# Kernel optimization log

Hardware: AMD Instinct MI355X
Metric: run time of the kernel (lower is better)

Reference implementation:

```python
import jax, jax.numpy as jnp
import numpy as np

N_NODES = 50000
N_EDGES = 600000
D_IN = 128
D_OUT = 128


def setup_inputs() -> dict:
    key = jax.random.key(0)
    k1, k2, k3, k4 = jax.random.split(key, 4)
    mpg_ft = jax.random.normal(k1, (N_NODES, D_IN), dtype=jnp.float32)
    edge_index = jax.random.randint(k2, (2, N_EDGES), 0, N_NODES, dtype=jnp.int64)
    # GCNConv linear params (PyG: glorot weight [in, out], zero bias)
    limit = (6.0 / (D_IN + D_OUT)) ** 0.5
    W = jax.random.uniform(k3, (D_IN, D_OUT), dtype=jnp.float32, minval=-limit, maxval=limit)
    b = jnp.zeros((D_OUT,), dtype=jnp.float32)
    return {"mpg_ft": mpg_ft, "edge_index": edge_index, "W": W, "b": b}


def gcn_conv(x, edge_index, W, b):
    n = x.shape[0]
    # add self-loops (PyG GCNConv default)
    loops = jnp.arange(n, dtype=edge_index.dtype)
    src = jnp.concatenate([edge_index[0], loops])
    dst = jnp.concatenate([edge_index[1], loops])
    # symmetric normalization: deg computed on destination with unit edge weights
    deg = jax.ops.segment_sum(jnp.ones_like(dst, dtype=x.dtype), dst, num_segments=n)
    dis = jnp.where(deg > 0, jax.lax.rsqrt(jnp.maximum(deg, 1.0)), 0.0)
    norm = dis[src] * dis[dst]                      # [E+N]
    h = x @ W                                        # [N, D_OUT]
    msg = h[src] * norm[:, None]                     # [E+N, D_OUT] gather
    out = jax.ops.segment_sum(msg, dst, num_segments=n)  # scatter-add
    return out + b


def reference(mpg_ft, edge_index, W, b):
    # freeze=True: x = g.mpg_ft; conv=True: x = GCNConv(x, edge_index)
    return gcn_conv(mpg_ft, edge_index, W, b)
```

## Files before the change

### kernel.cpp

```cpp
#include <hip/hip_runtime.h>

#define D 128
#define CAP 64
#define BINCAP 4096
#define BINSHIFT 8

typedef __bf16 bf16x8 __attribute__((ext_vector_type(8)));
typedef float f32x4 __attribute__((ext_vector_type(4)));

static __device__ __forceinline__ unsigned short f2bf(float x) {
    unsigned int u = __builtin_bit_cast(unsigned int, x);
    unsigned int r = u + 0x7fffu + ((u >> 16) & 1u);
    return (unsigned short)(r >> 16);
}
static __device__ __forceinline__ float bitf(unsigned int u) {
    return __builtin_bit_cast(float, u);
}

__global__ __launch_bounds__(256) void prep_kernel(const float* __restrict__ W,
                                                   unsigned int* __restrict__ bincur,
                                                   unsigned short* __restrict__ wt, int NB) {
    int tid = blockIdx.x * 256 + threadIdx.x;
    int stride = gridDim.x * 256;
    if (tid < NB) bincur[tid] = (unsigned)tid * BINCAP;
    for (int i = tid; i < D * D; i += stride) {
        int r = i >> 7, c = i & 127;
        wt[c * 128 + r] = f2bf(W[i]);
    }
}

__global__ __launch_bounds__(256) void binA_kernel(const int* __restrict__ ei,
                                                   unsigned int* __restrict__ bincur,
                                                   unsigned int* __restrict__ binned, int E,
                                                   int NB) {
    __shared__ unsigned int hist[256];
    __shared__ unsigned int base[256];
    int t = threadIdx.x;
    int chunk = (E + gridDim.x - 1) / gridDim.x;
    int s0 = blockIdx.x * chunk, s1 = min(E, s0 + chunk);
    const int* dstp = ei + E;

    hist[t] = 0u;
    __syncthreads();
    for (int e = s0 + t; e < s1; e += 256) atomicAdd(&hist[dstp[e] >> BINSHIFT], 1u);
    __syncthreads();
    if (t < NB && hist[t]) base[t] = atomicAdd(&bincur[t], hist[t]);
    __syncthreads();
    hist[t] = 0u;
    __syncthreads();
    for (int e = s0 + t; e < s1; e += 256) {
        int src = ei[e];
        int d = dstp[e];
        int bin = d >> BINSHIFT;
        unsigned int off = atomicAdd(&hist[bin], 1u);
        binned[base[bin] + off] = ((unsigned)d << 16) | (unsigned)src;
    }
}

__global__ __launch_bounds__(256) void binB_kernel(const unsigned int* __restrict__ binned,
                                                   const unsigned int* __restrict__ bincur,
                                                   unsigned int* __restrict__ cnt,
                                                   unsigned short* __restrict__ bucket, int n) {
    __shared__ unsigned int lcnt[256];
    int t = threadIdx.x;
    int b = blockIdx.x;
    lcnt[t] = 0u;
    __syncthreads();
    unsigned int cstart = (unsigned)b * BINCAP;
    int m = (int)(bincur[b] - cstart);
    for (int i = t; i < m; i += 256) {
        unsigned int p = binned[cstart + i];
        unsigned int src = p & 0xffffu;
        unsigned int d = p >> 16;
        unsigned int slot = atomicAdd(&lcnt[d & 255u], 1u);
        bucket[(size_t)d * CAP + (slot & (CAP - 1))] = (unsigned short)src;
    }
    __syncthreads();
    int node = (b << BINSHIFT) + t;
    if (node < n) cnt[node] = lcnt[t];
}

__global__ __launch_bounds__(256) void mfma_gemm(const float* __restrict__ x,
                                                 const unsigned short* __restrict__ wt,
                                                 const unsigned int* __restrict__ cnt,
                                                 unsigned short* __restrict__ hs, int n) {
    __shared__ uint4 Xs[64 * 16];
    __shared__ uint4 Ws[128 * 16];
    int t = threadIdx.x;
    int rowbase = blockIdx.x * 64;

    const uint4* wg = (const uint4*)wt;
#pragma unroll
    for (int j = 0; j < 8; ++j) {
        int gi = t + j * 256;
        int r = gi >> 4, s = gi & 15;
        Ws[r * 16 + (s ^ (r & 7))] = wg[gi];
    }
    const float4* x4 = (const float4*)x;
#pragma unroll
    for (int j = 0; j < 4; ++j) {
        int gi = t + j * 256;
        int r = gi >> 4, s = gi & 15;
        uint4 v = make_uint4(0u, 0u, 0u, 0u);
        int grow = rowbase + r;
        if (grow < n) {
            float4 f0 = x4[(size_t)grow * 32 + s * 2];
            float4 f1 = x4[(size_t)grow * 32 + s * 2 + 1];
            v.x = f2bf(f0.x) | ((unsigned)f2bf(f0.y) << 16);
            v.y = f2bf(f0.z) | ((unsigned)f2bf(f0.w) << 16);
            v.z = f2bf(f1.x) | ((unsigned)f2bf(f1.y) << 16);
            v.w = f2bf(f1.z) | ((unsigned)f2bf(f1.w) << 16);
        }
        Xs[r * 16 + (s ^ (r & 7))] = v;
    }
    __syncthreads();

    int w = t >> 6, l = t & 63;
    int lr = l & 15, lg = l >> 4;
    f32x4 acc[4][2] = {};

#pragma unroll
    for (int kt = 0; kt < 4; ++kt) {
        int ks = kt * 4 + lg;
        bf16x8 bfr[2];
#pragma unroll
        for (int ct = 0; ct < 2; ++ct) {
            int nc = w * 32 + ct * 16 + lr;
            bfr[ct] = __builtin_bit_cast(bf16x8, Ws[nc * 16 + (ks ^ (nc & 7))]);
        }
#pragma unroll
        for (int mt = 0; mt < 4; ++mt) {
            int mr = mt * 16 + lr;
            bf16x8 afr = __builtin_bit_cast(bf16x8, Xs[mr * 16 + (ks ^ (mr & 7))]);
            acc[mt][0] = __builtin_amdgcn_mfma_f32_16x16x32_bf16(afr, bfr[0], acc[mt][0], 0, 0, 0);
            acc[mt][1] = __builtin_amdgcn_mfma_f32_16x16x32_bf16(afr, bfr[1], acc[mt][1], 0, 0, 0);
        }
    }

#pragma unroll
    for (int mt = 0; mt < 4; ++mt) {
        int row0 = rowbase + mt * 16 + lg * 4;
#pragma unroll
        for (int r = 0; r < 4; ++r) {
            int grow = row0 + r;
            if (grow < n) {
                float dv = rsqrtf((float)cnt[grow] + 1.0f);
#pragma unroll
                for (int ct = 0; ct < 2; ++ct) {
                    int col = w * 32 + ct * 16 + lr;
                    hs[(size_t)grow * 128 + col] = f2bf(acc[mt][ct][r] * dv);
                }
            }
        }
    }
}

#define ACC8(A0, A1, U)                       \
    do {                                      \
        A0.x += bitf((U).x << 16);            \
        A0.y += bitf((U).x & 0xffff0000u);    \
        A0.z += bitf((U).y << 16);            \
        A0.w += bitf((U).y & 0xffff0000u);    \
        A1.x += bitf((U).z << 16);            \
        A1.y += bitf((U).z & 0xffff0000u);    \
        A1.z += bitf((U).w << 16);            \
        A1.w += bitf((U).w & 0xffff0000u);    \
    } while (0)

__global__ __launch_bounds__(256) void gather_kernel(const unsigned short* __restrict__ bucket,
                                                     const unsigned int* __restrict__ cnt,
                                                     const unsigned short* __restrict__ hs,
                                                     const float* __restrict__ b,
                                                     float* __restrict__ out, int n) {
    int node = (blockIdx.x * 256 + threadIdx.x) >> 4;
    int l = threadIdx.x & 15;
    if (node >= n) return;
    unsigned int c = cnt[node];
    const unsigned short* seg = bucket + (size_t)node * CAP;
    const uint4* h4 = (const uint4*)hs;

    uint4 u = h4[(size_t)node * 16 + l];
    float4 aA0 = make_float4(bitf(u.x << 16), bitf(u.x & 0xffff0000u), bitf(u.y << 16),
                             bitf(u.y & 0xffff0000u));
    float4 aA1 = make_float4(bitf(u.z << 16), bitf(u.z & 0xffff0000u), bitf(u.w << 16),
                             bitf(u.w & 0xffff0000u));
    float4 aB0 = make_float4(0.f, 0.f, 0.f, 0.f);
    float4 aB1 = make_float4(0.f, 0.f, 0.f, 0.f);

    for (unsigned int base = 0; base < c; base += 16) {
        int m = min(16u, c - base);
        int v = (l < m) ? (int)seg[base + l] : 0;
        int j = 0;
        for (; j + 3 < m; j += 4) {
            int s0 = __shfl(v, j, 16);
            int s1 = __shfl(v, j + 1, 16);
            int s2 = __shfl(v, j + 2, 16);
            int s3 = __shfl(v, j + 3, 16);
            uint4 u0 = h4[(size_t)s0 * 16 + l];
            uint4 u1 = h4[(size_t)s1 * 16 + l];
            uint4 u2 = h4[(size_t)s2 * 16 + l];
            uint4 u3 = h4[(size_t)s3 * 16 + l];
            ACC8(aA0, aA1, u0);
            ACC8(aB0, aB1, u1);
            ACC8(aA0, aA1, u2);
            ACC8(aB0, aB1, u3);
        }
        for (; j < m; ++j) {
            int s0 = __shfl(v, j, 16);
            uint4 u0 = h4[(size_t)s0 * 16 + l];
            ACC8(aA0, aA1, u0);
        }
    }

    float dd = rsqrtf((float)c + 1.0f);
    float4 bv0 = ((const float4*)b)[l * 2];
    float4 bv1 = ((const float4*)b)[l * 2 + 1];
    float4 r0 = make_float4((aA0.x + aB0.x) * dd + bv0.x, (aA0.y + aB0.y) * dd + bv0.y,
                            (aA0.z + aB0.z) * dd + bv0.z, (aA0.w + aB0.w) * dd + bv0.w);
    float4 r1 = make_float4((aA1.x + aB1.x) * dd + bv1.x, (aA1.y + aB1.y) * dd + bv1.y,
                            (aA1.z + aB1.z) * dd + bv1.z, (aA1.w + aB1.w) * dd + bv1.w);
    float4* o4 = (float4*)out;
    o4[(size_t)node * 32 + l * 2] = r0;
    o4[(size_t)node * 32 + l * 2 + 1] = r1;
}

extern "C" void kernel_launch(void* const* d_in, const int* in_sizes, int n_in,
                              void* d_out, int out_size, void* d_ws, size_t ws_size,
                              hipStream_t stream) {
    const float* x = (const float*)d_in[0];
    const int* ei = (const int*)d_in[1];
    const float* W = (const float*)d_in[2];
    const float* b = (const float*)d_in[3];
    float* out = (float*)d_out;

    int n = in_sizes[0] / D;
    int E = in_sizes[1] / 2;
    int NB = (n + 255) >> 8;

    unsigned int* bincur = (unsigned int*)d_ws;
    unsigned int* cnt = bincur + 256;
    unsigned int* binned = cnt + n;
    unsigned short* bucket = (unsigned short*)(binned + (size_t)NB * BINCAP);
    unsigned short* hs = bucket + (size_t)n * CAP;
    unsigned short* wt = hs + (size_t)n * D;

    prep_kernel<<<64, 256, 0, stream>>>(W, bincur, wt, NB);
    binA_kernel<<<128, 256, 0, stream>>>(ei, bincur, binned, E, NB);
    binB_kernel<<<NB, 256, 0, stream>>>(binned, bincur, cnt, bucket, n);
    mfma_gemm<<<(n + 63) / 64, 256, 0, stream>>>(x, wt, cnt, hs, n);
    gather_kernel<<<(n * 16 + 255) / 256, 256, 0, stream>>>(bucket, cnt, hs, b, out, n);
}
```

Before: 80.87 us.

## Fuse binning and GEMM launches, drop global bin cursor, move src normalization into gather

Cuts the pipeline from five kernel launches to three. The W transpose is merged into the first binning pass. The second binning pass and the MFMA GEMM run as disjoint block ranges of one launch. The global atomic bin cursor is replaced by fixed per-block sub-buckets sized from a per-block count table. Because the GEMM no longer depends on degrees, the source-side normalization moves into the gather, which reads a precomputed rsqrt degree array per neighbor. This trades fewer launch boundaries for an extra scalar load and multiply per edge, plus a fixed SUBCAP=64 per (bin, block) pair that could overflow on skewed inputs.

Measured after the change: 70.39 us. 13.0% less time.

```diff
diff --git a/kernel.cpp b/kernel.cpp
--- a/kernel.cpp
+++ b/kernel.cpp
@@ -2,7 +2,8 @@
 
 #define D 128
 #define CAP 64
-#define BINCAP 4096
+#define NBLK_A 128
+#define SUBCAP 64
 #define BINSHIFT 8
 
 typedef __bf16 bf16x8 __attribute__((ext_vector_type(8)));
@@ -17,77 +18,85 @@
     return __builtin_bit_cast(float, u);
 }
 
-__global__ __launch_bounds__(256) void prep_kernel(const float* __restrict__ W,
-                                                   unsigned int* __restrict__ bincur,
-                                                   unsigned short* __restrict__ wt, int NB) {
-    int tid = blockIdx.x * 256 + threadIdx.x;
-    int stride = gridDim.x * 256;
-    if (tid < NB) bincur[tid] = (unsigned)tid * BINCAP;
-    for (int i = tid; i < D * D; i += stride) {
-        int r = i >> 7, c = i & 127;
-        wt[c * 128 + r] = f2bf(W[i]);
-    }
-}
-
-__global__ __launch_bounds__(256) void binA_kernel(const int* __restrict__ ei,
-                                                   unsigned int* __restrict__ bincur,
-                                                   unsigned int* __restrict__ binned, int E,
-                                                   int NB) {
-    __shared__ unsigned int hist[256];
-    __shared__ unsigned int base[256];
+__global__ __launch_bounds__(256) void k1_kernel(const int* __restrict__ ei,
+                                                 const float* __restrict__ W,
+                                                 unsigned int* __restrict__ counts,
+                                                 unsigned int* __restrict__ binned,
+                                                 unsigned short* __restrict__ wt, int E) {
     int t = threadIdx.x;
-    int chunk = (E + gridDim.x - 1) / gridDim.x;
-    int s0 = blockIdx.x * chunk, s1 = min(E, s0 + chunk);
-    const int* dstp = ei + E;
-
-    hist[t] = 0u;
-    __syncthreads();
-    for (int e = s0 + t; e < s1; e += 256) atomicAdd(&hist[dstp[e] >> BINSHIFT], 1u);
-    __syncthreads();
-    if (t < NB && hist[t]) base[t] = atomicAdd(&bincur[t], hist[t]);
-    __syncthreads();
-    hist[t] = 0u;
-    __syncthreads();
-    for (int e = s0 + t; e < s1; e += 256) {
-        int src = ei[e];
-        int d = dstp[e];
-        int bin = d >> BINSHIFT;
-        unsigned int off = atomicAdd(&hist[bin], 1u);
-        binned[base[bin] + off] = ((unsigned)d << 16) | (unsigned)src;
-    }
-}
-
-__global__ __launch_bounds__(256) void binB_kernel(const unsigned int* __restrict__ binned,
-                                                   const unsigned int* __restrict__ bincur,
-                                                   unsigned int* __restrict__ cnt,
-                                                   unsigned short* __restrict__ bucket, int n) {
-    __shared__ unsigned int lcnt[256];
+    int k = blockIdx.x;
+    if (k < NBLK_A) {
+        __shared__ unsigned int hist[256];
+        hist[t] = 0u;
+        __syncthreads();
+        int chunk = (E + NBLK_A - 1) / NBLK_A;
+        int s0 = k * chunk, s1 = min(E, s0 + chunk);
+        const int* dstp = ei + E;
+        for (int e = s0 + t; e < s1; e += 256) atomicAdd(&hist[dstp[e] >> BINSHIFT], 1u);
+        __syncthreads();
+        counts[k * 256 + t] = hist[t];
+        __syncthreads();
+        hist[t] = 0u;
+        __syncthreads();
+        for (int e = s0 + t; e < s1; e += 256) {
+            int src = ei[e];
+            int d = dstp[e];
+            int bin = d >> BINSHIFT;
+            unsigned int off = atomicAdd(&hist[bin], 1u);
+            binned[((unsigned)bin * NBLK_A + (unsigned)k) * SUBCAP + off] =
+                ((unsigned)d << 16) | (unsigned)src;
+        }
+    } else {
+        int tid = (k - NBLK_A) * 256 + t;
+        for (int i = tid; i < D * D; i += 8 * 256) {
+            int r = i >> 7, c = i & 127;
+            wt[c * 128 + r] = f2bf(W[i]);
+        }
+    }
+}
+
+__global__ __launch_bounds__(256) void k2_kernel(const unsigned int* __restrict__ counts,
+                                                 const unsigned int* __restrict__ binned,
+                                                 const float* __restrict__ x,
+                                                 const unsigned short* __restrict__ wt,
+                                                 unsigned int* __restrict__ cnt,
+                                                 float* __restrict__ disf,
+                                                 unsigned short* __restrict__ bucket,
+                                                 unsigned short* __restrict__ hs, int n, int NB) {
+    __shared__ char smem[48 * 1024];
     int t = threadIdx.x;
-    int b = blockIdx.x;
-    lcnt[t] = 0u;
-    __syncthreads();
-    unsigned int cstart = (unsigned)b * BINCAP;
-    int m = (int)(bincur[b] - cstart);
-    for (int i = t; i < m; i += 256) {
-        unsigned int p = binned[cstart + i];
-        unsigned int src = p & 0xffffu;
-        unsigned int d = p >> 16;
-        unsigned int slot = atomicAdd(&lcnt[d & 255u], 1u);
-        bucket[(size_t)d * CAP + (slot & (CAP - 1))] = (unsigned short)src;
-    }
-    __syncthreads();
-    int node = (b << BINSHIFT) + t;
-    if (node < n) cnt[node] = lcnt[t];
-}
-
-__global__ __launch_bounds__(256) void mfma_gemm(const float* __restrict__ x,
-                                                 const unsigned short* __restrict__ wt,
-                                                 const unsigned int* __restrict__ cnt,
-                                                 unsigned short* __restrict__ hs, int n) {
-    __shared__ uint4 Xs[64 * 16];
-    __shared__ uint4 Ws[128 * 16];
-    int t = threadIdx.x;
-    int rowbase = blockIdx.x * 64;
+    int bid = blockIdx.x;
+
+    if (bid < NB) {
+        unsigned int* lcnt = (unsigned int*)smem;
+        lcnt[t] = 0u;
+        __syncthreads();
+        int wv = t >> 6, ln = t & 63;
+        int b = bid;
+        for (int k = wv; k < NBLK_A; k += 4) {
+            int m = (int)counts[k * 256 + b];
+            unsigned int base = ((unsigned)b * NBLK_A + (unsigned)k) * SUBCAP;
+            for (int i = ln; i < m; i += 64) {
+                unsigned int p = binned[base + i];
+                unsigned int d = p >> 16;
+                unsigned int src = p & 0xffffu;
+                unsigned int slot = atomicAdd(&lcnt[d & 255u], 1u);
+                bucket[(size_t)d * CAP + (slot & (CAP - 1))] = (unsigned short)src;
+            }
+        }
+        __syncthreads();
+        int node = (b << BINSHIFT) + t;
+        if (node < n) {
+            unsigned int c = lcnt[t];
+            cnt[node] = c;
+            disf[node] = rsqrtf((float)c + 1.0f);
+        }
+        return;
+    }
+
+    uint4* Xs = (uint4*)smem;
+    uint4* Ws = (uint4*)smem + 1024;
+    int rowbase = (bid - NB) * 64;
 
     const uint4* wg = (const uint4*)wt;
 #pragma unroll
@@ -144,31 +153,31 @@
         for (int r = 0; r < 4; ++r) {
             int grow = row0 + r;
             if (grow < n) {
-                float dv = rsqrtf((float)cnt[grow] + 1.0f);
 #pragma unroll
                 for (int ct = 0; ct < 2; ++ct) {
                     int col = w * 32 + ct * 16 + lr;
-                    hs[(size_t)grow * 128 + col] = f2bf(acc[mt][ct][r] * dv);
+                    hs[(size_t)grow * 128 + col] = f2bf(acc[mt][ct][r]);
                 }
             }
         }
     }
 }
 
-#define ACC8(A0, A1, U)                       \
-    do {                                      \
-        A0.x += bitf((U).x << 16);            \
-        A0.y += bitf((U).x & 0xffff0000u);    \
-        A0.z += bitf((U).y << 16);            \
-        A0.w += bitf((U).y & 0xffff0000u);    \
-        A1.x += bitf((U).z << 16);            \
-        A1.y += bitf((U).z & 0xffff0000u);    \
-        A1.z += bitf((U).w << 16);            \
-        A1.w += bitf((U).w & 0xffff0000u);    \
+#define ACC8F(A0, A1, U, DS)                       \
+    do {                                           \
+        A0.x += bitf((U).x << 16) * DS;            \
+        A0.y += bitf((U).x & 0xffff0000u) * DS;    \
+        A0.z += bitf((U).y << 16) * DS;            \
+        A0.w += bitf((U).y & 0xffff0000u) * DS;    \
+        A1.x += bitf((U).z << 16) * DS;            \
+        A1.y += bitf((U).z & 0xffff0000u) * DS;    \
+        A1.z += bitf((U).w << 16) * DS;            \
+        A1.w += bitf((U).w & 0xffff0000u) * DS;    \
     } while (0)
 
 __global__ __launch_bounds__(256) void gather_kernel(const unsigned short* __restrict__ bucket,
                                                      const unsigned int* __restrict__ cnt,
+                                                     const float* __restrict__ disf,
                                                      const unsigned short* __restrict__ hs,
                                                      const float* __restrict__ b,
                                                      float* __restrict__ out, int n) {
@@ -176,49 +185,59 @@
     int l = threadIdx.x & 15;
     if (node >= n) return;
     unsigned int c = cnt[node];
+    float dn = disf[node];
     const unsigned short* seg = bucket + (size_t)node * CAP;
     const uint4* h4 = (const uint4*)hs;
 
     uint4 u = h4[(size_t)node * 16 + l];
-    float4 aA0 = make_float4(bitf(u.x << 16), bitf(u.x & 0xffff0000u), bitf(u.y << 16),
-                             bitf(u.y & 0xffff0000u));
-    float4 aA1 = make_float4(bitf(u.z << 16), bitf(u.z & 0xffff0000u), bitf(u.w << 16),
-                             bitf(u.w & 0xffff0000u));
+    float4 aA0 = make_float4(bitf(u.x << 16) * dn, bitf(u.x & 0xffff0000u) * dn,
+                             bitf(u.y << 16) * dn, bitf(u.y & 0xffff0000u) * dn);
+    float4 aA1 = make_float4(bitf(u.z << 16) * dn, bitf(u.z & 0xffff0000u) * dn,
+                             bitf(u.w << 16) * dn, bitf(u.w & 0xffff0000u) * dn);
     float4 aB0 = make_float4(0.f, 0.f, 0.f, 0.f);
     float4 aB1 = make_float4(0.f, 0.f, 0.f, 0.f);
 
     for (unsigned int base = 0; base < c; base += 16) {
         int m = min(16u, c - base);
-        int v = (l < m) ? (int)seg[base + l] : 0;
+        int v = 0;
+        float dv = 0.f;
+        if (l < m) {
+            v = (int)seg[base + l];
+            dv = disf[v];
+        }
         int j = 0;
         for (; j + 3 < m; j += 4) {
             int s0 = __shfl(v, j, 16);
             int s1 = __shfl(v, j + 1, 16);
             int s2 = __shfl(v, j + 2, 16);
             int s3 = __shfl(v, j + 3, 16);
+            float d0 = __shfl(dv, j, 16);
+            float d1 = __shfl(dv, j + 1, 16);
+            float d2 = __shfl(dv, j + 2, 16);
+            float d3 = __shfl(dv, j + 3, 16);
             uint4 u0 = h4[(size_t)s0 * 16 + l];
             uint4 u1 = h4[(size_t)s1 * 16 + l];
             uint4 u2 = h4[(size_t)s2 * 16 + l];
             uint4 u3 = h4[(size_t)s3 * 16 + l];
-            ACC8(aA0, aA1, u0);
-            ACC8(aB0, aB1, u1);
-            ACC8(aA0, aA1, u2);
-            ACC8(aB0, aB1, u3);
+            ACC8F(aA0, aA1, u0, d0);
+            ACC8F(aB0, aB1, u1, d1);
+            ACC8F(aA0, aA1, u2, d2);
+            ACC8F(aB0, aB1, u3, d3);
         }
         for (; j < m; ++j) {
             int s0 = __shfl(v, j, 16);
+            float d0 = __shfl(dv, j, 16);
             uint4 u0 = h4[(size_t)s0 * 16 + l];
-            ACC8(aA0, aA1, u0);
-        }
-    }
-
-    float dd = rsqrtf((float)c + 1.0f);
+            ACC8F(aA0, aA1, u0, d0);
+        }
+    }
+
     float4 bv0 = ((const float4*)b)[l * 2];
     float4 bv1 = ((const float4*)b)[l * 2 + 1];
-    float4 r0 = make_float4((aA0.x + aB0.x) * dd + bv0.x, (aA0.y + aB0.y) * dd + bv0.y,
-                            (aA0.z + aB0.z) * dd + bv0.z, (aA0.w + aB0.w) * dd + bv0.w);
-    float4 r1 = make_float4((aA1.x + aB1.x) * dd + bv1.x, (aA1.y + aB1.y) * dd + bv1.y,
-                            (aA1.z + aB1.z) * dd + bv1.z, (aA1.w + aB1.w) * dd + bv1.w);
+    float4 r0 = make_float4((aA0.x + aB0.x) * dn + bv0.x, (aA0.y + aB0.y) * dn + bv0.y,
+                            (aA0.z + aB0.z) * dn + bv0.z, (aA0.w + aB0.w) * dn + bv0.w);
+    float4 r1 = make_float4((aA1.x + aB1.x) * dn + bv1.x, (aA1.y + aB1.y) * dn + bv1.y,
+                            (aA1.z + aB1.z) * dn + bv1.z, (aA1.w + aB1.w) * dn + bv1.w);
     float4* o4 = (float4*)out;
     o4[(size_t)node * 32 + l * 2] = r0;
     o4[(size_t)node * 32 + l * 2 + 1] = r1;
@@ -237,16 +256,16 @@
     int E = in_sizes[1] / 2;
     int NB = (n + 255) >> 8;
 
-    unsigned int* bincur = (unsigned int*)d_ws;
-    unsigned int* cnt = bincur + 256;
-    unsigned int* binned = cnt + n;
-    unsigned short* bucket = (unsigned short*)(binned + (size_t)NB * BINCAP);
+    unsigned int* counts = (unsigned int*)d_ws;
+    unsigned int* cnt = counts + NBLK_A * 256;
+    float* disf = (float*)(cnt + n);
+    unsigned int* binned = (unsigned int*)(disf + n);
+    unsigned short* bucket = (unsigned short*)(binned + (size_t)NB * NBLK_A * SUBCAP);
     unsigned short* hs = bucket + (size_t)n * CAP;
     unsigned short* wt = hs + (size_t)n * D;
 
-    prep_kernel<<<64, 256, 0, stream>>>(W, bincur, wt, NB);
-    binA_kernel<<<128, 256, 0, stream>>>(ei, bincur, binned, E, NB);
-    binB_kernel<<<NB, 256, 0, stream>>>(binned, bincur, cnt, bucket, n);
-    mfma_gemm<<<(n + 63) / 64, 256, 0, stream>>>(x, wt, cnt, hs, n);
-    gather_kernel<<<(n * 16 + 255) / 256, 256, 0, stream>>>(bucket, cnt, hs, b, out, n);
-}
+    k1_kernel<<<NBLK_A + 8, 256, 0, stream>>>(ei, W, counts, binned, wt, E);
+    k2_kernel<<<NB + (n + 63) / 64, 256, 0, stream>>>(counts, binned, x, wt, cnt, disf, bucket,
+                                                      hs, n, NB);
+    gather_kernel<<<(n * 16 + 255) / 256, 256, 0, stream>>>(bucket, cnt, disf, hs, b, out, n);
+}
```
